# Optimization experiments

Measured on AMD Instinct MI355X. Metric: run time of the kernel, lower is better.

## Reference

```python
import jax, jax.numpy as jnp
import numpy as np

B, S, H = 2, 2048, 2048
HEADS, G = 16, 4
HD = H // HEADS          # 128
M = HEADS // G           # query heads per KV group


def setup_inputs() -> dict:
    key = jax.random.key(0)
    ks = jax.random.split(key, 6)
    s = 0.02
    hidden_state = jax.random.normal(ks[0], (B, S, H), dtype=jnp.float32)
    attention_mask = jnp.ones((B, 1, 1, S), dtype=jnp.float32)
    Wq = jax.random.normal(ks[1], (H, H), dtype=jnp.float32) * s
    bq = jnp.zeros((H,), dtype=jnp.float32)
    Wk = jax.random.normal(ks[2], (H, G * HD), dtype=jnp.float32) * s
    bk = jnp.zeros((G * HD,), dtype=jnp.float32)
    Wv = jax.random.normal(ks[3], (H, G * HD), dtype=jnp.float32) * s
    bv = jnp.zeros((G * HD,), dtype=jnp.float32)
    Wo = jax.random.normal(ks[4], (H, H), dtype=jnp.float32) * s
    bo = jnp.zeros((H,), dtype=jnp.float32)
    return {"hidden_state": hidden_state, "attention_mask": attention_mask,
            "Wq": Wq, "bq": bq, "Wk": Wk, "bk": bk, "Wv": Wv, "bv": bv,
            "Wo": Wo, "bo": bo}


def reference(hidden_state, attention_mask, Wq, bq, Wk, bk, Wv, bv, Wo, bo):
    b, s, h = hidden_state.shape
    # projections
    q = hidden_state @ Wq + bq                      # (B,S,H)
    k = hidden_state @ Wk + bk                      # (B,S,G*HD)
    v = hidden_state @ Wv + bv                      # (B,S,G*HD)
    # split heads; query head ordering is group-major (head = g*M + m),
    # matching the original expand/reshape of K/V groups.
    q = q.reshape(b, s, HEADS, HD).transpose(0, 2, 1, 3).reshape(b, G, M, s, HD)
    k = k.reshape(b, s, G, HD).transpose(0, 2, 1, 3)  # (B,G,S,HD)
    v = v.reshape(b, s, G, HD).transpose(0, 2, 1, 3)  # (B,G,S,HD)
    # grouped attention: avoid materializing expanded K/V
    scale = 1.0 / jnp.sqrt(jnp.float32(HD))
    scores = jnp.einsum('bgmqd,bgkd->bgmqk', q, k) * scale  # (B,G,M,S,S)
    # faithful to source: scores += mask * -1e-9 (mask shape (B,1,1,S))
    scores = scores + attention_mask[:, :, :, None, :] * (-1e-9)
    probs = jax.nn.softmax(scores, axis=-1)
    out = jnp.einsum('bgmqk,bgkd->bgmqd', probs, v)          # (B,G,M,S,HD)
    out = out.reshape(b, HEADS, s, HD).transpose(0, 2, 1, 3).reshape(b, s, h)
    return out @ Wo + bo
```

## Files before the change

kernel.cpp:

```cpp
#include <hip/hip_runtime.h>
#include <cstdint>

typedef unsigned short u16;
typedef __attribute__((ext_vector_type(8))) short bf16x8;
typedef __attribute__((ext_vector_type(4))) float f32x4;

#define B_    2
#define S_    2048
#define H_    2048
#define G_    4
#define HD_   128
#define QKVW  3072

#define EXP2F(x) __builtin_amdgcn_exp2f(x)

__device__ __forceinline__ u16 f2bf(float f) {
  union { float f; unsigned u; } v; v.f = f;
  unsigned r = v.u + 0x7fffu + ((v.u >> 16) & 1u);
  return (u16)(r >> 16);
}

__device__ __forceinline__ void async16(void* lds_dst, const void* gsrc) {
  __builtin_amdgcn_global_load_lds(
      (__attribute__((address_space(1))) void*)gsrc,
      (__attribute__((address_space(3))) void*)lds_dst, 16, 0, 0);
}

__global__ __launch_bounds__(256)
void prelude_kernel(const float* __restrict__ X, u16* __restrict__ Xb,
                    const float* __restrict__ Wq, const float* __restrict__ Wk,
                    const float* __restrict__ Wv, const float* __restrict__ Wo,
                    u16* __restrict__ Wqkvt, u16* __restrict__ Wot)
{
  int id = blockIdx.x;
  if (id < 4096) {
    int i = id * 256 + threadIdx.x;
    const float4* p = (const float4*)X + (size_t)i * 2;
    float4 a = p[0], b = p[1];
    u16 h[8] = { f2bf(a.x), f2bf(a.y), f2bf(a.z), f2bf(a.w),
                 f2bf(b.x), f2bf(b.y), f2bf(b.z), f2bf(b.w) };
    *(uint4*)(Xb + (size_t)i * 8) = *(const uint4*)h;
    return;
  }
  id -= 4096;
  const float* W; u16* Wt; int Ndim, bx;
  if (id < 4096)      { W = Wq; Wt = Wqkvt;                        Ndim = 2048; bx = id;        }
  else if (id < 5120) { W = Wk; Wt = Wqkvt + (size_t)2048 * 2048;  Ndim = 512;  bx = id - 4096; }
  else if (id < 6144) { W = Wv; Wt = Wqkvt + (size_t)2560 * 2048;  Ndim = 512;  bx = id - 5120; }
  else                { W = Wo; Wt = Wot;                          Ndim = 2048; bx = id - 6144; }
  const int Kdim = 2048;
  const int nbx = Ndim >> 5;
  const int n0 = (bx % nbx) * 32, k0 = (bx / nbx) * 32;

  __shared__ float t[32][33];
  int tx = threadIdx.x & 31, ty = threadIdx.x >> 5;
#pragma unroll
  for (int j = 0; j < 4; ++j)
    t[ty + j * 8][tx] = W[(size_t)(k0 + ty + j * 8) * Ndim + n0 + tx];
  __syncthreads();
#pragma unroll
  for (int j = 0; j < 4; ++j)
    Wt[(size_t)(n0 + ty + j * 8) * Kdim + k0 + tx] = f2bf(t[tx][ty + j * 8]);
}

template <int MODE>
__global__ __launch_bounds__(512, 6)
void gemm_bt(const u16* __restrict__ A, const u16* __restrict__ Bt,
             const float* __restrict__ biasQ, const float* __restrict__ biasK,
             const float* __restrict__ biasV, void* __restrict__ Cout,
             u16* __restrict__ VtOut, int Ndim, int Kdim)
{
  __shared__ u16 As[128 * 64];
  __shared__ u16 Bs[128 * 64];
  const int tid  = threadIdx.x;
  const int lane = tid & 63;
  const int wv   = tid >> 6;

  const int wgid = blockIdx.x + gridDim.x * blockIdx.y;
  const int xcd  = wgid & 7;
  const int idx  = wgid >> 3;
  const int row0 = (xcd * 4 + (idx & 3)) * 128;
  const int col0 = (idx >> 2) * 128;

  const int wm = (wv >> 2) * 64;
  const int wn = (wv & 3) * 32;
  const int l15 = lane & 15, l4 = lane >> 4;

  f32x4 acc[4][2] = {};

  for (int kt = 0; kt < Kdim; kt += 64) {
    __syncthreads();
#pragma unroll
    for (int i = 0; i < 2; ++i) {
      int u = i * 512 + tid;
      int r = u >> 3, ci = u & 7;
      async16((char*)As + (i * 512 + wv * 64) * 16,
              A + (size_t)(row0 + r) * Kdim + kt + ci * 8);
    }
#pragma unroll
    for (int i = 0; i < 2; ++i) {
      int u = i * 512 + tid;
      int r = u >> 3, ci = u & 7;
      async16((char*)Bs + (i * 512 + wv * 64) * 16,
              Bt + (size_t)(col0 + r) * Kdim + kt + ci * 8);
    }
    __syncthreads();
#pragma unroll
    for (int ks = 0; ks < 2; ++ks) {
      bf16x8 af[4], bfr[2];
#pragma unroll
      for (int mt = 0; mt < 4; ++mt)
        af[mt] = *(const bf16x8*)&As[(wm + mt * 16 + l15) * 64 + ks * 32 + l4 * 8];
#pragma unroll
      for (int nt = 0; nt < 2; ++nt)
        bfr[nt] = *(const bf16x8*)&Bs[(wn + nt * 16 + l15) * 64 + ks * 32 + l4 * 8];
#pragma unroll
      for (int mt = 0; mt < 4; ++mt)
#pragma unroll
        for (int nt = 0; nt < 2; ++nt)
          acc[mt][nt] = __builtin_amdgcn_mfma_f32_16x16x32_bf16(af[mt], bfr[nt], acc[mt][nt], 0, 0, 0);
    }
  }

#pragma unroll
  for (int mt = 0; mt < 4; ++mt)
#pragma unroll
    for (int nt = 0; nt < 2; ++nt)
#pragma unroll
      for (int r = 0; r < 4; ++r) {
        int rr = row0 + wm + mt * 16 + l4 * 4 + r;
        int cc = col0 + wn + nt * 16 + l15;
        float bias;
        if (MODE == 3)
          bias = cc < 2048 ? biasQ[cc] : (cc < 2560 ? biasK[cc - 2048] : biasV[cc - 2560]);
        else
          bias = biasQ[cc];
        float v = acc[mt][nt][r] + bias;
        if (MODE == 1) {
          ((float*)Cout)[(size_t)rr * Ndim + cc] = v;
        } else {
          if (cc < 2048) v *= 0.12751743383412927f;
          if (cc < 2560) {
            ((u16*)Cout)[(size_t)rr * Ndim + cc] = f2bf(v);
          } else {
            int vc = cc - 2560;
            int gg = vc >> 7, d = vc & 127;
            VtOut[(((size_t)((rr >> 11) * G_ + gg)) * HD_ + d) * S_ + (rr & 2047)] = f2bf(v);
          }
        }
      }
}

__global__ __launch_bounds__(512, 2)
void attn_kernel(const u16* __restrict__ Qb, const u16* __restrict__ Kb,
                 const u16* __restrict__ Vt, u16* __restrict__ Ob)
{
  __shared__ u16 SH[40960];
  u16* Ps = SH + 24576;
  const int tid  = threadIdx.x;
  const int lane = tid & 63, wv = tid >> 6;
  const int l15 = lane & 15, l4 = lane >> 4;
  const int qt = blockIdx.x, head = blockIdx.y, b = blockIdx.z;
  const int g = head >> 2;
  const int s0 = qt * 256;

  bf16x8 qf[2][4];
  {
    const u16* qbase = Qb + ((size_t)(b * S_ + s0 + wv * 32 + l15)) * QKVW + head * HD_ + l4 * 8;
#pragma unroll
    for (int rg = 0; rg < 2; ++rg)
#pragma unroll
      for (int ks = 0; ks < 4; ++ks)
        qf[rg][ks] = *(const bf16x8*)(qbase + (size_t)rg * 16 * QKVW + ks * 32);
  }

  float m_r[2][4], lp[2][4];
#pragma unroll
  for (int rg = 0; rg < 2; ++rg)
#pragma unroll
    for (int r = 0; r < 4; ++r) { m_r[rg][r] = 0.f; lp[rg][r] = 0.f; }
  f32x4 aco[2][8] = {};

#define STAGE_K(buf, kt_)                                                      \
  _Pragma("unroll")                                                            \
  for (int i = 0; i < 2; ++i) {                                                \
    int u = i * 512 + tid;                                                     \
    int r = u >> 4;                                                            \
    int ci = (u & 15) ^ (r & 7);                                               \
    async16((char*)SH + (buf) * 16384 + (i * 512 + wv * 64) * 16,              \
            Kb + ((size_t)(b * S_ + (kt_) * 64 + r)) * QKVW + g * HD_ + ci * 8); \
  }
#define STAGE_V(kt_)                                                           \
  _Pragma("unroll")                                                            \
  for (int i = 0; i < 2; ++i) {                                                \
    int u = i * 512 + tid;                                                     \
    int r = u >> 3;                                                            \
    int ci = (u & 7) ^ (r & 7);                                                \
    async16((char*)SH + 32768 + (i * 512 + wv * 64) * 16,                      \
            Vt + (((size_t)(b * G_ + g)) * HD_ + r) * S_ + (kt_) * 64 + ci * 8); \
  }

  STAGE_K(0, 0);
  STAGE_V(0);
  __syncthreads();

  const u16* Vc = SH + 16384;
  int kcur = 0;
  for (int kt = 0; kt < S_ / 64; ++kt) {
    if (kt + 1 < S_ / 64) {
      STAGE_K(kcur ^ 1, kt + 1);
    }
    const u16* Kc = SH + kcur * 8192;

    f32x4 sc[2][4] = {};
    __builtin_amdgcn_s_setprio(1);
#pragma unroll
    for (int ct = 0; ct < 4; ++ct)
#pragma unroll
      for (int ks = 0; ks < 4; ++ks) {
        bf16x8 kf = *(const bf16x8*)&Kc[(ct * 16 + l15) * 128 + ((ks * 32 + l4 * 8) ^ ((l15 & 7) << 3))];
        sc[0][ct] = __builtin_amdgcn_mfma_f32_16x16x32_bf16(qf[0][ks], kf, sc[0][ct], 0, 0, 0);
        sc[1][ct] = __builtin_amdgcn_mfma_f32_16x16x32_bf16(qf[1][ks], kf, sc[1][ct], 0, 0, 0);
      }
    __builtin_amdgcn_s_setprio(0);

    float lm[2][4];
    bool resc = false;
#pragma unroll
    for (int rg = 0; rg < 2; ++rg)
#pragma unroll
      for (int r = 0; r < 4; ++r) {
        lm[rg][r] = fmaxf(fmaxf(sc[rg][0][r], sc[rg][1][r]),
                          fmaxf(sc[rg][2][r], sc[rg][3][r]));
        float d = lm[rg][r] - m_r[rg][r];
        resc |= (d > 8.0f) | (d < -60.0f);
      }
    if (__ballot(resc)) {
#pragma unroll
      for (int rg = 0; rg < 2; ++rg)
#pragma unroll
        for (int r = 0; r < 4; ++r) {
          float mx = lm[rg][r];
          mx = fmaxf(mx, __shfl_xor(mx, 1));
          mx = fmaxf(mx, __shfl_xor(mx, 2));
          mx = fmaxf(mx, __shfl_xor(mx, 4));
          mx = fmaxf(mx, __shfl_xor(mx, 8));
          float mn = fmaxf(m_r[rg][r], mx);
          float al = EXP2F(m_r[rg][r] - mn);
          m_r[rg][r] = mn;
          lp[rg][r] *= al;
#pragma unroll
          for (int dt = 0; dt < 8; ++dt)
            aco[rg][dt][r] *= al;
        }
    }

#pragma unroll
    for (int rg = 0; rg < 2; ++rg)
#pragma unroll
      for (int ct = 0; ct < 4; ++ct)
#pragma unroll
        for (int r = 0; r < 4; ++r) {
          float p = EXP2F(sc[rg][ct][r] - m_r[rg][r]);
          lp[rg][r] += p;
          int row = wv * 32 + rg * 16 + l4 * 4 + r;
          int col = ct * 16 + l15;
          Ps[row * 64 + (((col >> 3) ^ (row & 7)) << 3) + (col & 7)] = f2bf(p);
        }

    __syncthreads();

    __builtin_amdgcn_s_setprio(1);
#pragma unroll
    for (int k2 = 0; k2 < 2; ++k2) {
      bf16x8 pa0, pa1;
      {
        int pr0 = wv * 32 + l15;
        int pr1 = wv * 32 + 16 + l15;
        pa0 = *(const bf16x8*)&Ps[pr0 * 64 + (((k2 * 4 + l4) ^ (pr0 & 7)) << 3)];
        pa1 = *(const bf16x8*)&Ps[pr1 * 64 + (((k2 * 4 + l4) ^ (pr1 & 7)) << 3)];
      }
#pragma unroll
      for (int dt = 0; dt < 8; ++dt) {
        bf16x8 vf = *(const bf16x8*)&Vc[(dt * 16 + l15) * 64 + ((k2 * 32 + l4 * 8) ^ ((l15 & 7) << 3))];
        aco[0][dt] = __builtin_amdgcn_mfma_f32_16x16x32_bf16(pa0, vf, aco[0][dt], 0, 0, 0);
        aco[1][dt] = __builtin_amdgcn_mfma_f32_16x16x32_bf16(pa1, vf, aco[1][dt], 0, 0, 0);
      }
    }
    __builtin_amdgcn_s_setprio(0);

    __syncthreads();
    if (kt + 1 < S_ / 64) {
      STAGE_V(kt + 1);
    }
    kcur ^= 1;
  }
#undef STAGE_K
#undef STAGE_V

#pragma unroll
  for (int rg = 0; rg < 2; ++rg)
#pragma unroll
    for (int r = 0; r < 4; ++r) {
      float s = lp[rg][r];
      s += __shfl_xor(s, 1);
      s += __shfl_xor(s, 2);
      s += __shfl_xor(s, 4);
      s += __shfl_xor(s, 8);
      lp[rg][r] = 1.0f / s;
    }
#pragma unroll
  for (int rg = 0; rg < 2; ++rg)
#pragma unroll
    for (int dt = 0; dt < 8; ++dt)
#pragma unroll
      for (int r = 0; r < 4; ++r) {
        int srow = s0 + wv * 32 + rg * 16 + l4 * 4 + r;
        int col = head * HD_ + dt * 16 + l15;
        Ob[((size_t)(b * S_ + srow)) * H_ + col] = f2bf(aco[rg][dt][r] * lp[rg][r]);
      }
}

extern "C" void kernel_launch(void* const* d_in, const int* in_sizes, int n_in,
                              void* d_out, int out_size, void* d_ws, size_t ws_size,
                              hipStream_t stream)
{
  const float* X    = (const float*)d_in[0];
  const float* Wq   = (const float*)d_in[2];
  const float* bq   = (const float*)d_in[3];
  const float* Wk   = (const float*)d_in[4];
  const float* bk   = (const float*)d_in[5];
  const float* Wv   = (const float*)d_in[6];
  const float* bv   = (const float*)d_in[7];
  const float* Wo   = (const float*)d_in[8];
  const float* bo   = (const float*)d_in[9];
  float* out = (float*)d_out;

  char* ws = (char*)d_ws;
  u16* Xb    = (u16*)(ws + 0);
  u16* QKV   = (u16*)(ws + (16u << 20));
  u16* Vt    = (u16*)(ws + (40u << 20));
  u16* Ab    = (u16*)(ws + (44u << 20));
  u16* Wqkvt = (u16*)(ws + (60u << 20));
  u16* Wot   = (u16*)(ws + (72u << 20));

  const u16* Qb = QKV;
  const u16* Kb = QKV + 2048;

  prelude_kernel<<<dim3(14336), 256, 0, stream>>>(X, Xb, Wq, Wk, Wv, Wo, Wqkvt, Wot);

  gemm_bt<3><<<dim3(32, 24), 512, 0, stream>>>(Xb, Wqkvt, bq, bk, bv, QKV, Vt, QKVW, 2048);

  attn_kernel<<<dim3(8, 16, 2), 512, 0, stream>>>(Qb, Kb, Vt, Ab);

  gemm_bt<1><<<dim3(32, 16), 512, 0, stream>>>(Ab, Wot, bo, nullptr, nullptr, out, nullptr, 2048, 2048);
}
```

Measured before the change: 244.9 us.

## Split attention over two KV halves and merge with weighted combine kernel

Measured after the change: 259.8 us. 1.06x slower.

```diff
diff --git a/kernel.cpp b/kernel.cpp
--- a/kernel.cpp
+++ b/kernel.cpp
@@ -18,6 +18,10 @@
   union { float f; unsigned u; } v; v.f = f;
   unsigned r = v.u + 0x7fffu + ((v.u >> 16) & 1u);
   return (u16)(r >> 16);
+}
+
+__device__ __forceinline__ float bf2f(u16 h) {
+  union { unsigned u; float f; } v; v.u = ((unsigned)h) << 16; return v.f;
 }
 
 __device__ __forceinline__ void async16(void* lds_dst, const void* gsrc) {
@@ -153,16 +157,20 @@
 
 __global__ __launch_bounds__(512, 2)
 void attn_kernel(const u16* __restrict__ Qb, const u16* __restrict__ Kb,
-                 const u16* __restrict__ Vt, u16* __restrict__ Ob)
+                 const u16* __restrict__ Vt, u16* __restrict__ O0,
+                 u16* __restrict__ O1, float* __restrict__ Wbuf)
 {
   __shared__ u16 SH[40960];
   u16* Ps = SH + 24576;
   const int tid  = threadIdx.x;
   const int lane = tid & 63, wv = tid >> 6;
   const int l15 = lane & 15, l4 = lane >> 4;
-  const int qt = blockIdx.x, head = blockIdx.y, b = blockIdx.z;
+  const int qt = blockIdx.x, head = blockIdx.y;
+  const int b = blockIdx.z >> 1, shalf = blockIdx.z & 1;
   const int g = head >> 2;
   const int s0 = qt * 256;
+  const int kt0 = shalf * 16;
+  u16* Oh = shalf ? O1 : O0;
 
   bf16x8 qf[2][4];
   {
@@ -200,17 +208,17 @@
             Vt + (((size_t)(b * G_ + g)) * HD_ + r) * S_ + (kt_) * 64 + ci * 8); \
   }
 
-  STAGE_K(0, 0);
-  STAGE_V(0);
+  STAGE_K(0, kt0);
+  STAGE_V(kt0);
   __syncthreads();
 
   const u16* Vc = SH + 16384;
-  int kcur = 0;
-  for (int kt = 0; kt < S_ / 64; ++kt) {
-    if (kt + 1 < S_ / 64) {
-      STAGE_K(kcur ^ 1, kt + 1);
-    }
-    const u16* Kc = SH + kcur * 8192;
+  int kc = 0;
+  for (int kt = kt0; kt < kt0 + 16; ++kt) {
+    if (kt + 1 < kt0 + 16) {
+      STAGE_K(kc ^ 1, kt + 1);
+    }
+    const u16* Kc = SH + kc * 8192;
 
     f32x4 sc[2][4] = {};
     __builtin_amdgcn_s_setprio(1);
@@ -290,10 +298,10 @@
     __builtin_amdgcn_s_setprio(0);
 
     __syncthreads();
-    if (kt + 1 < S_ / 64) {
+    if (kt + 1 < kt0 + 16) {
       STAGE_V(kt + 1);
     }
-    kcur ^= 1;
+    kc ^= 1;
   }
 #undef STAGE_K
 #undef STAGE_V
@@ -307,6 +315,10 @@
       s += __shfl_xor(s, 2);
       s += __shfl_xor(s, 4);
       s += __shfl_xor(s, 8);
+      if (l15 == 0) {
+        int srow = s0 + wv * 32 + rg * 16 + l4 * 4 + r;
+        Wbuf[((size_t)(shalf * (B_ * S_) + b * S_ + srow)) * 16 + head] = s * EXP2F(m_r[rg][r]);
+      }
       lp[rg][r] = 1.0f / s;
     }
 #pragma unroll
@@ -317,8 +329,32 @@
       for (int r = 0; r < 4; ++r) {
         int srow = s0 + wv * 32 + rg * 16 + l4 * 4 + r;
         int col = head * HD_ + dt * 16 + l15;
-        Ob[((size_t)(b * S_ + srow)) * H_ + col] = f2bf(aco[rg][dt][r] * lp[rg][r]);
-      }
+        Oh[((size_t)(b * S_ + srow)) * H_ + col] = f2bf(aco[rg][dt][r] * lp[rg][r]);
+      }
+}
+
+__global__ __launch_bounds__(256)
+void combine_kernel(u16* __restrict__ O0, const u16* __restrict__ O1,
+                    const float* __restrict__ Wbuf)
+{
+  int t = blockIdx.x * 256 + threadIdx.x;
+  int row = t >> 8;
+  int c0  = (t & 255) * 8;
+  int head = c0 >> 7;
+  float w0 = Wbuf[(size_t)row * 16 + head];
+  float w1 = Wbuf[(size_t)(B_ * S_ + row) * 16 + head];
+  float inv = 1.0f / (w0 + w1);
+  w0 *= inv; w1 *= inv;
+  size_t idx = (size_t)row * H_ + c0;
+  uint4 a = *(const uint4*)&O0[idx];
+  uint4 bb = *(const uint4*)&O1[idx];
+  const u16* pa = (const u16*)&a;
+  const u16* pb = (const u16*)&bb;
+  u16 h[8];
+#pragma unroll
+  for (int j = 0; j < 8; ++j)
+    h[j] = f2bf(w0 * bf2f(pa[j]) + w1 * bf2f(pb[j]));
+  *(uint4*)&O0[idx] = *(const uint4*)h;
 }
 
 extern "C" void kernel_launch(void* const* d_in, const int* in_sizes, int n_in,
@@ -343,6 +379,7 @@
   u16* Ab    = (u16*)(ws + (44u << 20));
   u16* Wqkvt = (u16*)(ws + (60u << 20));
   u16* Wot   = (u16*)(ws + (72u << 20));
+  float* Wbuf = (float*)(ws + (60u << 20));
 
   const u16* Qb = QKV;
   const u16* Kb = QKV + 2048;
@@ -351,7 +388,9 @@
 
   gemm_bt<3><<<dim3(32, 24), 512, 0, stream>>>(Xb, Wqkvt, bq, bk, bv, QKV, Vt, QKVW, 2048);
 
-  attn_kernel<<<dim3(8, 16, 2), 512, 0, stream>>>(Qb, Kb, Vt, Ab);
+  attn_kernel<<<dim3(8, 16, 4), 512, 0, stream>>>(Qb, Kb, Vt, Ab, Xb, Wbuf);
+
+  combine_kernel<<<dim3(4096), 256, 0, stream>>>(Ab, Xb, Wbuf);
 
   gemm_bt<1><<<dim3(32, 16), 512, 0, stream>>>(Ab, Wot, bo, nullptr, nullptr, out, nullptr, 2048, 2048);
 }
```
